# Performance work log

Hardware: AMD Instinct MI355X
Metric: run time of the kernel (lower is better)

The kernel has to match this reference:

```python
import jax, jax.numpy as jnp
import numpy as np
from jax import lax

TAU = 2.0      # LIF decay constant (source: tau = 2.0)
V_TH = 1.0     # spikingjelly LIFNode default threshold
ALPHA = 2.0    # ATan surrogate default alpha
BN_EPS = 1e-5


@jax.custom_vjp
def spike(v):
    # Heaviside with ATan surrogate gradient (spikingjelly surrogate.ATan)
    return (v >= V_TH).astype(v.dtype)

def _spike_fwd(v):
    return spike(v), v

def _spike_bwd(v, g):
    x = (jnp.pi / 2.0) * ALPHA * (v - V_TH)
    return (g * (ALPHA / 2.0) / (1.0 + x * x),)

spike.defvjp(_spike_fwd, _spike_bwd)


def lif_step(v, x):
    # leaky integrate: v += (x - (v - v_reset)) / tau, v_reset = 0
    v = v + (x - v) / TAU
    s = spike(v)
    # hard reset to 0; detach_reset=True -> stop_gradient on s in the reset path
    v = v * (1.0 - lax.stop_gradient(s))
    return v, s


def multistep_lif(x_seq):
    # x_seq: (T, ...) ; membrane state carried across T, initial v = 0
    v0 = jnp.zeros_like(x_seq[0])
    _, s_seq = lax.scan(lif_step, v0, x_seq)
    return s_seq


def setup_inputs() -> dict:
    key = jax.random.key(0)
    ks = jax.random.split(key, 3)
    bs, length, c_num, hidden = 64, 128, 32, 256
    x = jax.random.normal(ks[0], (bs, length, c_num), dtype=jnp.float32)
    conv_w = jax.random.normal(ks[1], (hidden, 1, 1, 3), dtype=jnp.float32) * 0.3
    conv_b = jnp.zeros((hidden,), jnp.float32)
    bn_gamma = jnp.ones((hidden,), jnp.float32)
    bn_beta = jnp.zeros((hidden,), jnp.float32)
    bn_mean = jnp.zeros((hidden,), jnp.float32)
    bn_var = jnp.ones((hidden,), jnp.float32)
    lin_w = jax.random.normal(ks[2], (hidden, hidden), dtype=jnp.float32) * (1.0 / np.sqrt(hidden))
    lin_b = jnp.zeros((hidden,), jnp.float32)
    return {"x": x, "conv_w": conv_w, "conv_b": conv_b, "bn_gamma": bn_gamma,
            "bn_beta": bn_beta, "bn_mean": bn_mean, "bn_var": bn_var,
            "lin_w": lin_w, "lin_b": lin_b}


def reference(x, conv_w, conv_b, bn_gamma, bn_beta, bn_mean, bn_var, lin_w, lin_b):
    bs, length, c_num = x.shape
    hidden = conv_w.shape[0]

    # ---- ConvEncoder ----
    xi = jnp.transpose(x, (0, 2, 1))[:, None]  # (bs, 1, c_num, length)
    enc = lax.conv_general_dilated(
        xi, conv_w, window_strides=(1, 1), padding=((0, 0), (1, 1)),
        dimension_numbers=("NCHW", "OIHW", "NCHW"))
    enc = enc + conv_b[None, :, None, None]
    # BatchNorm2d (eval mode, running stats)
    inv = bn_gamma * lax.rsqrt(bn_var + BN_EPS)
    enc = (enc - bn_mean[None, :, None, None]) * inv[None, :, None, None] + bn_beta[None, :, None, None]
    # multi-step LIF over channel dim T = hidden (as in source permute(1,0,2,3))
    enc = jnp.transpose(enc, (1, 0, 2, 3))          # (hidden, bs, c_num, length)
    spks_enc = multistep_lif(enc)                   # (hidden, bs, c_num, length)

    # ---- reshape to per-(bs*c_num) sequences of length `length` with feature hidden ----
    h = jnp.transpose(spks_enc, (1, 2, 3, 0)).reshape(bs * c_num, length, hidden)

    # ---- SpikeRNNCell recurrence over time (Linear + stateful LIF) ----
    def rnn_step(v, x_t):                           # x_t: (N, hidden)
        z = x_t @ lin_w.T + lin_b
        v = v + (z - v) / TAU
        s = spike(v)
        v = v * (1.0 - lax.stop_gradient(s))
        return v, s

    v0 = jnp.zeros((bs * c_num, hidden), x.dtype)
    _, s_seq = lax.scan(rnn_step, v0, jnp.transpose(h, (1, 0, 2)))  # (length, N, hidden)
    spks = s_seq[-1]                                # final-step spikes (N, hidden)

    spks = spks.reshape(bs, c_num * hidden, -1)     # (bs, c_num*hidden, 1)
    return jnp.transpose(spks, (0, 2, 1)), spks[:, :, -1]
```

## Files before the change

kernel.cpp:

```cpp
#include <hip/hip_runtime.h>
#include <stdint.h>

typedef unsigned short u16;
typedef unsigned int u32;
typedef unsigned long long u64;
typedef unsigned char u8;

typedef __attribute__((ext_vector_type(4))) int   i32x4;
typedef __attribute__((ext_vector_type(8))) int   i32x8;
typedef __attribute__((ext_vector_type(4))) float f32x4;
typedef __attribute__((ext_vector_type(2))) float f32x2;

#define OFF_SBITS 0u
#define SBITS_BYTES (2048u * 128u * 32u)
#define OFF_WQ4  (SBITS_BYTES)
#define WQ4_BYTES (2u * 32768u)
#define OFF_SCL  (OFF_WQ4 + WQ4_BYTES)

__device__ __forceinline__ f32x2 pk_fma(f32x2 a, f32x2 b, f32x2 c) {
    f32x2 d;
    asm("v_pk_fma_f32 %0, %1, %2, %3"
        : "=v"(d) : "v"(a), "v"(b), "v"(c));
    return d;
}
__device__ __forceinline__ f32x2 pk_fma_lw(f32x2 a, f32x2 b) {
    f32x2 d;
    asm("v_pk_fma_f32 %0, %1, %2, %1 op_sel:[0,0,1] op_sel_hi:[0,1,1]"
        : "=v"(d) : "v"(a), "v"(b));
    return d;
}
__device__ __forceinline__ f32x2 pk_fma_b11(f32x2 a, f32x2 b, f32x2 c) {
    f32x2 d;
    asm("v_pk_fma_f32 %0, %1, %2, %3 op_sel:[1,0,0] op_sel_hi:[1,1,1]"
        : "=v"(d) : "v"(a), "v"(b), "v"(c));
    return d;
}
__device__ __forceinline__ f32x2 pk_fma_b00(f32x2 a, f32x2 b, f32x2 c) {
    f32x2 d;
    asm("v_pk_fma_f32 %0, %1, %2, %3 op_sel:[0,0,0] op_sel_hi:[0,1,1]"
        : "=v"(d) : "v"(a), "v"(b), "v"(c));
    return d;
}

__global__ __launch_bounds__(256) void prep_enc_kernel(
    const float* __restrict__ x,
    const float* __restrict__ conv_w, const float* __restrict__ conv_b,
    const float* __restrict__ gamma,  const float* __restrict__ beta,
    const float* __restrict__ mean,   const float* __restrict__ var,
    const float* __restrict__ lin_w,  uint8_t* __restrict__ ws,
    u32* __restrict__ sbits) {
    int tid = threadIdx.x;
    int blk = blockIdx.x;
    if (blk < 256) {
        __shared__ float red[256];
        __shared__ u8 nib[256];
        int j = blk, k = tid;
        float wv = lin_w[j * 256 + k];
        red[k] = fabsf(wv);
        __syncthreads();
        #pragma unroll
        for (int s = 128; s > 0; s >>= 1) {
            if (k < s) red[k] = fmaxf(red[k], red[k + s]);
            __syncthreads();
        }
        float m = red[0];
        float S = (m > 0.f) ? 6.0f / m : 0.f;
        float v6 = wv * S;
        float av = fabsf(v6);
        int code;
        if      (av < 0.25f) code = 0;
        else if (av < 0.75f) code = 1;
        else if (av < 1.25f) code = 2;
        else if (av < 1.75f) code = 3;
        else if (av < 2.5f)  code = 4;
        else if (av < 3.5f)  code = 5;
        else if (av < 5.0f)  code = 6;
        else                 code = 7;
        nib[k] = (u8)(((v6 < 0.f && code) ? 8 : 0) | code);
        __syncthreads();
        if (k < 128) {
            u8 byte = (u8)(nib[2 * k] | (nib[2 * k + 1] << 4));
            int ks = k >> 6, kb = (k >> 4) & 3, bi = k & 15;
            (ws + OFF_WQ4)[ks * 32768 + (j * 4 + kb) * 16 + bi] = byte;
        }
        if (k == 0) ((float*)(ws + OFF_SCL))[j] = m * (1.0f / 12.0f);
    } else {
        __shared__ f32x4 cfl[256];
        {
            int h = tid;
            float inv = gamma[h] / sqrtf(var[h] + 1e-5f);
            float K = (conv_b[h] - mean[h]) * inv + beta[h];
            f32x4 cc = {conv_w[h * 3 + 0] * inv * 0.5f,
                        conv_w[h * 3 + 1] * inv * 0.5f,
                        conv_w[h * 3 + 2] * inv * 0.5f, K * 0.5f};
            cfl[h] = cc;
        }
        int p = (blk - 256) * 256 + tid;
        int l = p & 127;
        int c = (p >> 7) & 31;
        int b0 = p >> 12;
        int xb = b0 * 4096 + l * 32 + c;
        float xb0 = x[xb],            xb1 = x[xb + 131072];
        float xa0 = (l > 0)   ? x[xb - 32]          : 0.f;
        float xa1 = (l > 0)   ? x[xb + 131072 - 32] : 0.f;
        float xc0 = (l < 127) ? x[xb + 32]          : 0.f;
        float xc1 = (l < 127) ? x[xb + 131072 + 32] : 0.f;
        u32* d0 = sbits + (size_t)(b0 * 32 + c) * 1024 + l;
        u32* d1 = d0 + (size_t)1024 * 1024;

        f32x2 XA = {xa0, xa1};
        f32x2 XB = {xb0, xb1};
        f32x2 XC = {xc0, xc1};
        const f32x2 hf2 = {0.5f, 0.5f};

        __syncthreads();
        f32x2 v2 = {0.f, 0.f};
        #pragma unroll 1
        for (int hc = 0; hc < 8; ++hc) {
            u32 c0 = 0, c1 = 0;
            #pragma unroll
            for (int k = 0; k < 32; ++k) {
                f32x4 a4 = cfl[hc * 32 + k];
                f32x2 p0 = __builtin_shufflevector(a4, a4, 0, 1);
                f32x2 p1 = __builtin_shufflevector(a4, a4, 2, 3);
                f32x2 e = pk_fma_lw(p1, XC);
                e = pk_fma_b11(p0, XB, e);
                e = pk_fma_b00(p0, XA, e);
                v2 = pk_fma(hf2, v2, e);
                bool s0 = (v2.x >= 1.0f);
                bool s1 = (v2.y >= 1.0f);
                c0 = (c0 << 1) | (u32)s0;
                c1 = (c1 << 1) | (u32)s1;
                v2.x = s0 ? 0.f : v2.x;
                v2.y = s1 ? 0.f : v2.y;
            }
            d0[hc * 128] = __builtin_bitreverse32(c0);
            d1[hc * 128] = __builtin_bitreverse32(c1);
        }
    }
}

__device__ __forceinline__ u32 nib_perm(u32 byte) {
    u32 t1 = byte | (byte << 6);
    u32 t2 = t1 | (t1 << 12);
    u32 sel = t2 & 0x03030303u;
    return __builtin_amdgcn_perm(0x22200200u, 0x22200200u, sel);
}

__global__ __launch_bounds__(256, 2) void gemm_scan_kernel(
    const u32* __restrict__ sbits,
    const uint4* __restrict__ wq4,
    const float* __restrict__ lin_b,
    const float* __restrict__ sclp,
    float* __restrict__ out) {
    __shared__ __align__(16) uint8_t smem[36864];
    u32* Awords = (u32*)smem;

    int tid  = threadIdx.x;
    int n    = blockIdx.x;
    int lane = tid & 63;
    int w    = tid >> 6;
    int l15  = lane & 15;
    int quad = lane >> 4;
    int lb   = w * 256 + l15 * 4 + quad;

    float bias = lin_b[tid];
    float zscg = fmaxf(sclp[tid], 1e-37f);
    float uth  = (1.0f - bias) / zscg;
    float urst = (0.0f - bias) / zscg;

    i32x4 bb[2][4];
    #pragma unroll
    for (int ks = 0; ks < 2; ++ks)
        #pragma unroll
        for (int nf = 0; nf < 4; ++nf)
            bb[ks][nf] = ((const i32x4*)wq4)[(size_t)(ks * 2048 + nf * 64 + lb)];

    __builtin_amdgcn_global_load_lds(
        (const __attribute__((address_space(1))) u32*)
            (sbits + (size_t)n * 1024 + tid * 4),
        (__attribute__((address_space(3))) u32*)(smem + w * 1024), 16, 0, 0);

    f32x4 acc[8][4];
    #pragma unroll
    for (int mf = 0; mf < 8; ++mf)
        #pragma unroll
        for (int nf = 0; nf < 4; ++nf) {
            f32x4 z = {0.f, 0.f, 0.f, 0.f};
            acc[mf][nf] = z;
        }

    __syncthreads();

    u32 aw[8][2];
    #pragma unroll
    for (int mf = 0; mf < 8; ++mf)
        #pragma unroll
        for (int ks = 0; ks < 2; ++ks)
            aw[mf][ks] = Awords[(ks * 4 + quad) * 128 + mf * 16 + l15];

    __syncthreads();

    i32x8 afr;
    afr[4] = 0; afr[5] = 0; afr[6] = 0; afr[7] = 0;

    #pragma unroll
    for (int ks = 0; ks < 2; ++ks) {
        i32x8 bfr[4];
        #pragma unroll
        for (int nf = 0; nf < 4; ++nf) {
            bfr[nf][0] = bb[ks][nf][0]; bfr[nf][1] = bb[ks][nf][1];
            bfr[nf][2] = bb[ks][nf][2]; bfr[nf][3] = bb[ks][nf][3];
            bfr[nf][4] = 0; bfr[nf][5] = 0; bfr[nf][6] = 0; bfr[nf][7] = 0;
        }
        #pragma unroll
        for (int mf = 0; mf < 8; ++mf) {
            u32 wbits = aw[mf][ks];
            afr[0] = (int)nib_perm(wbits & 0xFFu);
            afr[1] = (int)nib_perm((wbits >> 8) & 0xFFu);
            afr[2] = (int)nib_perm((wbits >> 16) & 0xFFu);
            afr[3] = (int)nib_perm(wbits >> 24);
            #pragma unroll
            for (int nf = 0; nf < 4; ++nf) {
                acc[mf][nf] = __builtin_amdgcn_mfma_scale_f32_16x16x128_f8f6f4(
                    afr, bfr[nf], acc[mf][nf], 4, 4,
                    0, 0x7F7F7F7F, 0, 0x7F7F7F7F);
            }
        }
    }

    float* ZW = (float*)(smem + (size_t)w * 9216);
    float u = urst, sOut = 0.f;
    #pragma unroll
    for (int ph = 0; ph < 4; ++ph) {
        #pragma unroll
        for (int mm = 0; mm < 2; ++mm) {
            int mf = ph * 2 + mm;
            #pragma unroll
            for (int nf = 0; nf < 4; ++nf)
                *(f32x4*)(ZW + (nf * 16 + l15) * 36 + mm * 16 + quad * 4) =
                    acc[mf][nf];
        }
        #pragma unroll
        for (int g = 0; g < 8; ++g) {
            f32x4 z4 = *(const f32x4*)(ZW + lane * 36 + g * 4);
            #pragma unroll
            for (int r = 0; r < 4; ++r) {
                u = fmaf(0.5f, u, z4[r]);
                bool s = (u >= uth);
                if (ph == 3 && g == 7 && r == 3) sOut = s ? 1.f : 0.f;
                u = s ? urst : u;
            }
        }
    }
    out[(size_t)n * 256 + tid]           = sOut;
    out[524288u + (size_t)n * 256 + tid] = sOut;
}

extern "C" void kernel_launch(void* const* d_in, const int* in_sizes, int n_in,
                              void* d_out, int out_size, void* d_ws, size_t ws_size,
                              hipStream_t stream) {
    const float* x      = (const float*)d_in[0];
    const float* conv_w = (const float*)d_in[1];
    const float* conv_b = (const float*)d_in[2];
    const float* gamma  = (const float*)d_in[3];
    const float* beta   = (const float*)d_in[4];
    const float* mean   = (const float*)d_in[5];
    const float* var    = (const float*)d_in[6];
    const float* lin_w  = (const float*)d_in[7];
    const float* lin_b  = (const float*)d_in[8];
    uint8_t* ws = (uint8_t*)d_ws;
    float* out = (float*)d_out;

    hipLaunchKernelGGL(prep_enc_kernel, dim3(768), dim3(256), 0, stream,
                       x, conv_w, conv_b, gamma, beta, mean, var, lin_w,
                       ws, (u32*)(ws + OFF_SBITS));
    hipLaunchKernelGGL(gemm_scan_kernel, dim3(2048), dim3(256), 0, stream,
                       (const u32*)(ws + OFF_SBITS),
                       (const uint4*)(ws + OFF_WQ4), lin_b,
                       (const float*)(ws + OFF_SCL), out);
}
```

Baseline: 111.2 us.

## Pre-expand spike bits to fp4 MFMA fragment layout in encoder kernel

The encoder kernel now expands each 32-bit spike word into 16 bytes of packed fp4 nibbles and writes them in the exact per-lane MFMA A-fragment layout. The GEMM kernel then loads 16 KB per block via four global-to-LDS loads and reads fragments directly, dropping the nib_perm unpacking from the GEMM inner loop. The cost is four times more workspace traffic: the spike buffer grows from 8 MB to 32 MB, written once and read once.

```diff
diff --git a/kernel.cpp b/kernel.cpp
--- a/kernel.cpp
+++ b/kernel.cpp
@@ -12,7 +12,7 @@
 typedef __attribute__((ext_vector_type(2))) float f32x2;
 
 #define OFF_SBITS 0u
-#define SBITS_BYTES (2048u * 128u * 32u)
+#define SBITS_BYTES (2048u * 16384u)
 #define OFF_WQ4  (SBITS_BYTES)
 #define WQ4_BYTES (2u * 32768u)
 #define OFF_SCL  (OFF_WQ4 + WQ4_BYTES)
@@ -40,6 +40,13 @@
     asm("v_pk_fma_f32 %0, %1, %2, %3 op_sel:[0,0,0] op_sel_hi:[0,1,1]"
         : "=v"(d) : "v"(a), "v"(b), "v"(c));
     return d;
+}
+
+__device__ __forceinline__ u32 nib_perm(u32 byte) {
+    u32 t1 = byte | (byte << 6);
+    u32 t2 = t1 | (t1 << 12);
+    u32 sel = t2 & 0x03030303u;
+    return __builtin_amdgcn_perm(0x22200200u, 0x22200200u, sel);
 }
 
 __global__ __launch_bounds__(256) void prep_enc_kernel(
@@ -48,7 +55,7 @@
     const float* __restrict__ gamma,  const float* __restrict__ beta,
     const float* __restrict__ mean,   const float* __restrict__ var,
     const float* __restrict__ lin_w,  uint8_t* __restrict__ ws,
-    u32* __restrict__ sbits) {
+    uint8_t* __restrict__ sbits) {
     int tid = threadIdx.x;
     int blk = blockIdx.x;
     if (blk < 256) {
@@ -105,8 +112,9 @@
         float xa1 = (l > 0)   ? x[xb + 131072 - 32] : 0.f;
         float xc0 = (l < 127) ? x[xb + 32]          : 0.f;
         float xc1 = (l < 127) ? x[xb + 131072 + 32] : 0.f;
-        u32* d0 = sbits + (size_t)(b0 * 32 + c) * 1024 + l;
-        u32* d1 = d0 + (size_t)1024 * 1024;
+        u8* base0 = sbits + (size_t)(b0 * 32 + c) * 16384
+                          + (size_t)(l >> 4) * 1024 + (size_t)(l & 15) * 16;
+        u8* base1 = base0 + (size_t)1024 * 16384;
 
         f32x2 XA = {xa0, xa1};
         f32x2 XB = {xb0, xb1};
@@ -134,27 +142,31 @@
                 v2.x = s0 ? 0.f : v2.x;
                 v2.y = s1 ? 0.f : v2.y;
             }
-            d0[hc * 128] = __builtin_bitreverse32(c0);
-            d1[hc * 128] = __builtin_bitreverse32(c1);
+            u32 w0 = __builtin_bitreverse32(c0);
+            u32 w1 = __builtin_bitreverse32(c1);
+            i32x4 e0, e1;
+            e0[0] = (int)nib_perm(w0 & 0xFFu);
+            e0[1] = (int)nib_perm((w0 >> 8) & 0xFFu);
+            e0[2] = (int)nib_perm((w0 >> 16) & 0xFFu);
+            e0[3] = (int)nib_perm(w0 >> 24);
+            e1[0] = (int)nib_perm(w1 & 0xFFu);
+            e1[1] = (int)nib_perm((w1 >> 8) & 0xFFu);
+            e1[2] = (int)nib_perm((w1 >> 16) & 0xFFu);
+            e1[3] = (int)nib_perm(w1 >> 24);
+            int off = (hc >> 2) * 8192 + (hc & 3) * 256;
+            *(i32x4*)(base0 + off) = e0;
+            *(i32x4*)(base1 + off) = e1;
         }
     }
 }
 
-__device__ __forceinline__ u32 nib_perm(u32 byte) {
-    u32 t1 = byte | (byte << 6);
-    u32 t2 = t1 | (t1 << 12);
-    u32 sel = t2 & 0x03030303u;
-    return __builtin_amdgcn_perm(0x22200200u, 0x22200200u, sel);
-}
-
 __global__ __launch_bounds__(256, 2) void gemm_scan_kernel(
-    const u32* __restrict__ sbits,
+    const uint8_t* __restrict__ sbits,
     const uint4* __restrict__ wq4,
     const float* __restrict__ lin_b,
     const float* __restrict__ sclp,
     float* __restrict__ out) {
     __shared__ __align__(16) uint8_t smem[36864];
-    u32* Awords = (u32*)smem;
 
     int tid  = threadIdx.x;
     int n    = blockIdx.x;
@@ -176,10 +188,13 @@
         for (int nf = 0; nf < 4; ++nf)
             bb[ks][nf] = ((const i32x4*)wq4)[(size_t)(ks * 2048 + nf * 64 + lb)];
 
-    __builtin_amdgcn_global_load_lds(
-        (const __attribute__((address_space(1))) u32*)
-            (sbits + (size_t)n * 1024 + tid * 4),
-        (__attribute__((address_space(3))) u32*)(smem + w * 1024), 16, 0, 0);
+    #pragma unroll
+    for (int j = 0; j < 4; ++j)
+        __builtin_amdgcn_global_load_lds(
+            (const __attribute__((address_space(1))) u32*)
+                (sbits + (size_t)n * 16384 + j * 4096 + tid * 16),
+            (__attribute__((address_space(3))) u32*)(smem + j * 4096 + w * 1024),
+            16, 0, 0);
 
     f32x4 acc[8][4];
     #pragma unroll
@@ -192,17 +207,12 @@
 
     __syncthreads();
 
-    u32 aw[8][2];
-    #pragma unroll
-    for (int mf = 0; mf < 8; ++mf)
-        #pragma unroll
-        for (int ks = 0; ks < 2; ++ks)
-            aw[mf][ks] = Awords[(ks * 4 + quad) * 128 + mf * 16 + l15];
+    i32x4 A4[16];
+    #pragma unroll
+    for (int f = 0; f < 16; ++f)
+        A4[f] = *(const i32x4*)(smem + f * 1024 + lane * 16);
 
     __syncthreads();
-
-    i32x8 afr;
-    afr[4] = 0; afr[5] = 0; afr[6] = 0; afr[7] = 0;
 
     #pragma unroll
     for (int ks = 0; ks < 2; ++ks) {
@@ -215,11 +225,10 @@
         }
         #pragma unroll
         for (int mf = 0; mf < 8; ++mf) {
-            u32 wbits = aw[mf][ks];
-            afr[0] = (int)nib_perm(wbits & 0xFFu);
-            afr[1] = (int)nib_perm((wbits >> 8) & 0xFFu);
-            afr[2] = (int)nib_perm((wbits >> 16) & 0xFFu);
-            afr[3] = (int)nib_perm(wbits >> 24);
+            i32x4 a4 = A4[ks * 8 + mf];
+            i32x8 afr;
+            afr[0] = a4[0]; afr[1] = a4[1]; afr[2] = a4[2]; afr[3] = a4[3];
+            afr[4] = 0; afr[5] = 0; afr[6] = 0; afr[7] = 0;
             #pragma unroll
             for (int nf = 0; nf < 4; ++nf) {
                 acc[mf][nf] = __builtin_amdgcn_mfma_scale_f32_16x16x128_f8f6f4(
@@ -274,9 +283,9 @@
 
     hipLaunchKernelGGL(prep_enc_kernel, dim3(768), dim3(256), 0, stream,
                        x, conv_w, conv_b, gamma, beta, mean, var, lin_w,
-                       ws, (u32*)(ws + OFF_SBITS));
+                       ws, ws + OFF_SBITS);
     hipLaunchKernelGGL(gemm_scan_kernel, dim3(2048), dim3(256), 0, stream,
-                       (const u32*)(ws + OFF_SBITS),
+                       ws + OFF_SBITS,
                        (const uint4*)(ws + OFF_WQ4), lin_b,
                        (const float*)(ws + OFF_SCL), out);
 }
```

Result: slower. 119.5 us (+7.5%).

## Fuse encoder LIF spike generation into the GEMM-scan kernel via shared memory

Applied to the files above, without the earlier changes.

The conv+BN+LIF encoder, which produced spike bitmasks, now runs inside the GEMM/scan kernel. Each block builds the spike bits for four (batch, channel) sequences in shared memory and then runs the FP4 MFMA GEMM and the recurrent LIF scan over them in a loop. This removes the 8 MB global round trip for the spike bits. The price is 512 blocks instead of 2048, more shared memory per block (57 KB), and each block doing four GEMM passes serially, which may lower occupancy and parallelism.

```diff
diff --git a/kernel.cpp b/kernel.cpp
--- a/kernel.cpp
+++ b/kernel.cpp
@@ -11,9 +11,7 @@
 typedef __attribute__((ext_vector_type(4))) float f32x4;
 typedef __attribute__((ext_vector_type(2))) float f32x2;
 
-#define OFF_SBITS 0u
-#define SBITS_BYTES (2048u * 128u * 32u)
-#define OFF_WQ4  (SBITS_BYTES)
+#define OFF_WQ4  0u
 #define WQ4_BYTES (2u * 32768u)
 #define OFF_SCL  (OFF_WQ4 + WQ4_BYTES)
 
@@ -40,104 +38,6 @@
     asm("v_pk_fma_f32 %0, %1, %2, %3 op_sel:[0,0,0] op_sel_hi:[0,1,1]"
         : "=v"(d) : "v"(a), "v"(b), "v"(c));
     return d;
-}
-
-__global__ __launch_bounds__(256) void prep_enc_kernel(
-    const float* __restrict__ x,
-    const float* __restrict__ conv_w, const float* __restrict__ conv_b,
-    const float* __restrict__ gamma,  const float* __restrict__ beta,
-    const float* __restrict__ mean,   const float* __restrict__ var,
-    const float* __restrict__ lin_w,  uint8_t* __restrict__ ws,
-    u32* __restrict__ sbits) {
-    int tid = threadIdx.x;
-    int blk = blockIdx.x;
-    if (blk < 256) {
-        __shared__ float red[256];
-        __shared__ u8 nib[256];
-        int j = blk, k = tid;
-        float wv = lin_w[j * 256 + k];
-        red[k] = fabsf(wv);
-        __syncthreads();
-        #pragma unroll
-        for (int s = 128; s > 0; s >>= 1) {
-            if (k < s) red[k] = fmaxf(red[k], red[k + s]);
-            __syncthreads();
-        }
-        float m = red[0];
-        float S = (m > 0.f) ? 6.0f / m : 0.f;
-        float v6 = wv * S;
-        float av = fabsf(v6);
-        int code;
-        if      (av < 0.25f) code = 0;
-        else if (av < 0.75f) code = 1;
-        else if (av < 1.25f) code = 2;
-        else if (av < 1.75f) code = 3;
-        else if (av < 2.5f)  code = 4;
-        else if (av < 3.5f)  code = 5;
-        else if (av < 5.0f)  code = 6;
-        else                 code = 7;
-        nib[k] = (u8)(((v6 < 0.f && code) ? 8 : 0) | code);
-        __syncthreads();
-        if (k < 128) {
-            u8 byte = (u8)(nib[2 * k] | (nib[2 * k + 1] << 4));
-            int ks = k >> 6, kb = (k >> 4) & 3, bi = k & 15;
-            (ws + OFF_WQ4)[ks * 32768 + (j * 4 + kb) * 16 + bi] = byte;
-        }
-        if (k == 0) ((float*)(ws + OFF_SCL))[j] = m * (1.0f / 12.0f);
-    } else {
-        __shared__ f32x4 cfl[256];
-        {
-            int h = tid;
-            float inv = gamma[h] / sqrtf(var[h] + 1e-5f);
-            float K = (conv_b[h] - mean[h]) * inv + beta[h];
-            f32x4 cc = {conv_w[h * 3 + 0] * inv * 0.5f,
-                        conv_w[h * 3 + 1] * inv * 0.5f,
-                        conv_w[h * 3 + 2] * inv * 0.5f, K * 0.5f};
-            cfl[h] = cc;
-        }
-        int p = (blk - 256) * 256 + tid;
-        int l = p & 127;
-        int c = (p >> 7) & 31;
-        int b0 = p >> 12;
-        int xb = b0 * 4096 + l * 32 + c;
-        float xb0 = x[xb],            xb1 = x[xb + 131072];
-        float xa0 = (l > 0)   ? x[xb - 32]          : 0.f;
-        float xa1 = (l > 0)   ? x[xb + 131072 - 32] : 0.f;
-        float xc0 = (l < 127) ? x[xb + 32]          : 0.f;
-        float xc1 = (l < 127) ? x[xb + 131072 + 32] : 0.f;
-        u32* d0 = sbits + (size_t)(b0 * 32 + c) * 1024 + l;
-        u32* d1 = d0 + (size_t)1024 * 1024;
-
-        f32x2 XA = {xa0, xa1};
-        f32x2 XB = {xb0, xb1};
-        f32x2 XC = {xc0, xc1};
-        const f32x2 hf2 = {0.5f, 0.5f};
-
-        __syncthreads();
-        f32x2 v2 = {0.f, 0.f};
-        #pragma unroll 1
-        for (int hc = 0; hc < 8; ++hc) {
-            u32 c0 = 0, c1 = 0;
-            #pragma unroll
-            for (int k = 0; k < 32; ++k) {
-                f32x4 a4 = cfl[hc * 32 + k];
-                f32x2 p0 = __builtin_shufflevector(a4, a4, 0, 1);
-                f32x2 p1 = __builtin_shufflevector(a4, a4, 2, 3);
-                f32x2 e = pk_fma_lw(p1, XC);
-                e = pk_fma_b11(p0, XB, e);
-                e = pk_fma_b00(p0, XA, e);
-                v2 = pk_fma(hf2, v2, e);
-                bool s0 = (v2.x >= 1.0f);
-                bool s1 = (v2.y >= 1.0f);
-                c0 = (c0 << 1) | (u32)s0;
-                c1 = (c1 << 1) | (u32)s1;
-                v2.x = s0 ? 0.f : v2.x;
-                v2.y = s1 ? 0.f : v2.y;
-            }
-            d0[hc * 128] = __builtin_bitreverse32(c0);
-            d1[hc * 128] = __builtin_bitreverse32(c1);
-        }
-    }
 }
 
 __device__ __forceinline__ u32 nib_perm(u32 byte) {
@@ -147,17 +47,56 @@
     return __builtin_amdgcn_perm(0x22200200u, 0x22200200u, sel);
 }
 
-__global__ __launch_bounds__(256, 2) void gemm_scan_kernel(
-    const u32* __restrict__ sbits,
+__global__ __launch_bounds__(256) void prep_kernel(
+    const float* __restrict__ lin_w, uint8_t* __restrict__ ws) {
+    __shared__ float red[256];
+    __shared__ u8 nib[256];
+    int j = blockIdx.x, k = threadIdx.x;
+    float wv = lin_w[j * 256 + k];
+    red[k] = fabsf(wv);
+    __syncthreads();
+    #pragma unroll
+    for (int s = 128; s > 0; s >>= 1) {
+        if (k < s) red[k] = fmaxf(red[k], red[k + s]);
+        __syncthreads();
+    }
+    float m = red[0];
+    float S = (m > 0.f) ? 6.0f / m : 0.f;
+    float v6 = wv * S;
+    float av = fabsf(v6);
+    int code;
+    if      (av < 0.25f) code = 0;
+    else if (av < 0.75f) code = 1;
+    else if (av < 1.25f) code = 2;
+    else if (av < 1.75f) code = 3;
+    else if (av < 2.5f)  code = 4;
+    else if (av < 3.5f)  code = 5;
+    else if (av < 5.0f)  code = 6;
+    else                 code = 7;
+    nib[k] = (u8)(((v6 < 0.f && code) ? 8 : 0) | code);
+    __syncthreads();
+    if (k < 128) {
+        u8 byte = (u8)(nib[2 * k] | (nib[2 * k + 1] << 4));
+        int ks = k >> 6, kb = (k >> 4) & 3, bi = k & 15;
+        (ws + OFF_WQ4)[ks * 32768 + (j * 4 + kb) * 16 + bi] = byte;
+    }
+    if (k == 0) ((float*)(ws + OFF_SCL))[j] = m * (1.0f / 12.0f);
+}
+
+__global__ __launch_bounds__(256, 2) void enc_gemm_kernel(
+    const float* __restrict__ x,
+    const float* __restrict__ conv_w, const float* __restrict__ conv_b,
+    const float* __restrict__ gamma,  const float* __restrict__ beta,
+    const float* __restrict__ mean,   const float* __restrict__ var,
     const uint4* __restrict__ wq4,
-    const float* __restrict__ lin_b,
-    const float* __restrict__ sclp,
+    const float* __restrict__ lin_b,  const float* __restrict__ sclp,
     float* __restrict__ out) {
-    __shared__ __align__(16) uint8_t smem[36864];
-    u32* Awords = (u32*)smem;
+    __shared__ __align__(16) uint8_t smem[57344];
+    u32*   bits = (u32*)smem;
+    f32x4* cfl  = (f32x4*)(smem + 16384);
 
     int tid  = threadIdx.x;
-    int n    = blockIdx.x;
+    int blk  = blockIdx.x;
     int lane = tid & 63;
     int w    = tid >> 6;
     int l15  = lane & 15;
@@ -176,85 +115,140 @@
         for (int nf = 0; nf < 4; ++nf)
             bb[ks][nf] = ((const i32x4*)wq4)[(size_t)(ks * 2048 + nf * 64 + lb)];
 
-    __builtin_amdgcn_global_load_lds(
-        (const __attribute__((address_space(1))) u32*)
-            (sbits + (size_t)n * 1024 + tid * 4),
-        (__attribute__((address_space(3))) u32*)(smem + w * 1024), 16, 0, 0);
-
-    f32x4 acc[8][4];
-    #pragma unroll
-    for (int mf = 0; mf < 8; ++mf)
-        #pragma unroll
-        for (int nf = 0; nf < 4; ++nf) {
-            f32x4 z = {0.f, 0.f, 0.f, 0.f};
-            acc[mf][nf] = z;
+    {
+        int h = tid;
+        float inv = gamma[h] / sqrtf(var[h] + 1e-5f);
+        float K = (conv_b[h] - mean[h]) * inv + beta[h];
+        f32x4 cc = {conv_w[h * 3 + 0] * inv * 0.5f,
+                    conv_w[h * 3 + 1] * inv * 0.5f,
+                    conv_w[h * 3 + 2] * inv * 0.5f, K * 0.5f};
+        cfl[h] = cc;
+    }
+
+    int l     = tid & 127;
+    int chalf = tid >> 7;
+    int cpair = (blk * 2) & 31;
+    int c     = cpair + chalf;
+    int b0    = blk >> 4;
+    int xb = b0 * 4096 + l * 32 + c;
+    float xb0 = x[xb],            xb1 = x[xb + 131072];
+    float xa0 = (l > 0)   ? x[xb - 32]          : 0.f;
+    float xa1 = (l > 0)   ? x[xb + 131072 - 32] : 0.f;
+    float xc0 = (l < 127) ? x[xb + 32]          : 0.f;
+    float xc1 = (l < 127) ? x[xb + 131072 + 32] : 0.f;
+    u32* d0 = bits + chalf * 1024 + l;
+    u32* d1 = d0 + 2 * 1024;
+
+    f32x2 XA = {xa0, xa1};
+    f32x2 XB = {xb0, xb1};
+    f32x2 XC = {xc0, xc1};
+    const f32x2 hf2 = {0.5f, 0.5f};
+
+    __syncthreads();
+    f32x2 v2 = {0.f, 0.f};
+    #pragma unroll 1
+    for (int hc = 0; hc < 8; ++hc) {
+        u32 c0 = 0, c1 = 0;
+        #pragma unroll
+        for (int k = 0; k < 32; ++k) {
+            f32x4 a4 = cfl[hc * 32 + k];
+            f32x2 p0 = __builtin_shufflevector(a4, a4, 0, 1);
+            f32x2 p1 = __builtin_shufflevector(a4, a4, 2, 3);
+            f32x2 e = pk_fma_lw(p1, XC);
+            e = pk_fma_b11(p0, XB, e);
+            e = pk_fma_b00(p0, XA, e);
+            v2 = pk_fma(hf2, v2, e);
+            bool s0 = (v2.x >= 1.0f);
+            bool s1 = (v2.y >= 1.0f);
+            c0 = (c0 << 1) | (u32)s0;
+            c1 = (c1 << 1) | (u32)s1;
+            v2.x = s0 ? 0.f : v2.x;
+            v2.y = s1 ? 0.f : v2.y;
         }
-
-    __syncthreads();
-
-    u32 aw[8][2];
-    #pragma unroll
-    for (int mf = 0; mf < 8; ++mf)
-        #pragma unroll
-        for (int ks = 0; ks < 2; ++ks)
-            aw[mf][ks] = Awords[(ks * 4 + quad) * 128 + mf * 16 + l15];
-
-    __syncthreads();
-
-    i32x8 afr;
-    afr[4] = 0; afr[5] = 0; afr[6] = 0; afr[7] = 0;
-
-    #pragma unroll
-    for (int ks = 0; ks < 2; ++ks) {
-        i32x8 bfr[4];
-        #pragma unroll
-        for (int nf = 0; nf < 4; ++nf) {
-            bfr[nf][0] = bb[ks][nf][0]; bfr[nf][1] = bb[ks][nf][1];
-            bfr[nf][2] = bb[ks][nf][2]; bfr[nf][3] = bb[ks][nf][3];
-            bfr[nf][4] = 0; bfr[nf][5] = 0; bfr[nf][6] = 0; bfr[nf][7] = 0;
+        d0[hc * 128] = __builtin_bitreverse32(c0);
+        d1[hc * 128] = __builtin_bitreverse32(c1);
+    }
+
+    __syncthreads();
+
+    float* ZW = (float*)(smem + 20480 + (size_t)w * 9216);
+    const u32* bp = bits + quad * 128 + l15;
+
+    #pragma unroll 1
+    for (int s = 0; s < 4; ++s) {
+        int n = b0 * 32 + cpair + (s & 1) + (s >> 1) * 1024;
+
+        u32 aw[8][2];
+        #pragma unroll
+        for (int mf = 0; mf < 8; ++mf)
+            #pragma unroll
+            for (int ks = 0; ks < 2; ++ks)
+                aw[mf][ks] = bp[s * 1024 + ks * 512 + mf * 16];
+
+        f32x4 acc[8][4];
+        #pragma unroll
+        for (int mf = 0; mf < 8; ++mf)
+            #pragma unroll
+            for (int nf = 0; nf < 4; ++nf) {
+                f32x4 z = {0.f, 0.f, 0.f, 0.f};
+                acc[mf][nf] = z;
+            }
+
+        i32x8 afr;
+        afr[4] = 0; afr[5] = 0; afr[6] = 0; afr[7] = 0;
+
+        #pragma unroll
+        for (int ks = 0; ks < 2; ++ks) {
+            i32x8 bfr[4];
+            #pragma unroll
+            for (int nf = 0; nf < 4; ++nf) {
+                bfr[nf][0] = bb[ks][nf][0]; bfr[nf][1] = bb[ks][nf][1];
+                bfr[nf][2] = bb[ks][nf][2]; bfr[nf][3] = bb[ks][nf][3];
+                bfr[nf][4] = 0; bfr[nf][5] = 0; bfr[nf][6] = 0; bfr[nf][7] = 0;
+            }
+            #pragma unroll
+            for (int mf = 0; mf < 8; ++mf) {
+                u32 wbits = aw[mf][ks];
+                afr[0] = (int)nib_perm(wbits & 0xFFu);
+                afr[1] = (int)nib_perm((wbits >> 8) & 0xFFu);
+                afr[2] = (int)nib_perm((wbits >> 16) & 0xFFu);
+                afr[3] = (int)nib_perm(wbits >> 24);
+                #pragma unroll
+                for (int nf = 0; nf < 4; ++nf) {
+                    acc[mf][nf] =
+                        __builtin_amdgcn_mfma_scale_f32_16x16x128_f8f6f4(
+                            afr, bfr[nf], acc[mf][nf], 4, 4,
+                            0, 0x7F7F7F7F, 0, 0x7F7F7F7F);
+                }
+            }
         }
-        #pragma unroll
-        for (int mf = 0; mf < 8; ++mf) {
-            u32 wbits = aw[mf][ks];
-            afr[0] = (int)nib_perm(wbits & 0xFFu);
-            afr[1] = (int)nib_perm((wbits >> 8) & 0xFFu);
-            afr[2] = (int)nib_perm((wbits >> 16) & 0xFFu);
-            afr[3] = (int)nib_perm(wbits >> 24);
-            #pragma unroll
-            for (int nf = 0; nf < 4; ++nf) {
-                acc[mf][nf] = __builtin_amdgcn_mfma_scale_f32_16x16x128_f8f6f4(
-                    afr, bfr[nf], acc[mf][nf], 4, 4,
-                    0, 0x7F7F7F7F, 0, 0x7F7F7F7F);
+
+        float u = urst, sOut = 0.f;
+        #pragma unroll
+        for (int ph = 0; ph < 4; ++ph) {
+            #pragma unroll
+            for (int mm = 0; mm < 2; ++mm) {
+                int mf = ph * 2 + mm;
+                #pragma unroll
+                for (int nf = 0; nf < 4; ++nf)
+                    *(f32x4*)(ZW + (nf * 16 + l15) * 36 + mm * 16 + quad * 4) =
+                        acc[mf][nf];
+            }
+            #pragma unroll
+            for (int g = 0; g < 8; ++g) {
+                f32x4 z4 = *(const f32x4*)(ZW + lane * 36 + g * 4);
+                #pragma unroll
+                for (int r = 0; r < 4; ++r) {
+                    u = fmaf(0.5f, u, z4[r]);
+                    bool sp = (u >= uth);
+                    if (ph == 3 && g == 7 && r == 3) sOut = sp ? 1.f : 0.f;
+                    u = sp ? urst : u;
+                }
             }
         }
-    }
-
-    float* ZW = (float*)(smem + (size_t)w * 9216);
-    float u = urst, sOut = 0.f;
-    #pragma unroll
-    for (int ph = 0; ph < 4; ++ph) {
-        #pragma unroll
-        for (int mm = 0; mm < 2; ++mm) {
-            int mf = ph * 2 + mm;
-            #pragma unroll
-            for (int nf = 0; nf < 4; ++nf)
-                *(f32x4*)(ZW + (nf * 16 + l15) * 36 + mm * 16 + quad * 4) =
-                    acc[mf][nf];
-        }
-        #pragma unroll
-        for (int g = 0; g < 8; ++g) {
-            f32x4 z4 = *(const f32x4*)(ZW + lane * 36 + g * 4);
-            #pragma unroll
-            for (int r = 0; r < 4; ++r) {
-                u = fmaf(0.5f, u, z4[r]);
-                bool s = (u >= uth);
-                if (ph == 3 && g == 7 && r == 3) sOut = s ? 1.f : 0.f;
-                u = s ? urst : u;
-            }
-        }
-    }
-    out[(size_t)n * 256 + tid]           = sOut;
-    out[524288u + (size_t)n * 256 + tid] = sOut;
+        out[(size_t)n * 256 + tid]           = sOut;
+        out[524288u + (size_t)n * 256 + tid] = sOut;
+    }
 }
 
 extern "C" void kernel_launch(void* const* d_in, const int* in_sizes, int n_in,
@@ -272,11 +266,10 @@
     uint8_t* ws = (uint8_t*)d_ws;
     float* out = (float*)d_out;
 
-    hipLaunchKernelGGL(prep_enc_kernel, dim3(768), dim3(256), 0, stream,
-                       x, conv_w, conv_b, gamma, beta, mean, var, lin_w,
-                       ws, (u32*)(ws + OFF_SBITS));
-    hipLaunchKernelGGL(gemm_scan_kernel, dim3(2048), dim3(256), 0, stream,
-                       (const u32*)(ws + OFF_SBITS),
+    hipLaunchKernelGGL(prep_kernel, dim3(256), dim3(256), 0, stream,
+                       lin_w, ws);
+    hipLaunchKernelGGL(enc_gemm_kernel, dim3(512), dim3(256), 0, stream,
+                       x, conv_w, conv_b, gamma, beta, mean, var,
                        (const uint4*)(ws + OFF_WQ4), lin_b,
                        (const float*)(ws + OFF_SCL), out);
 }
```

Measured after the change: 107.7 us. 1.03x faster.
